# Optimization experiments

Hardware: AMD Instinct MI355X
Metric: run time of the kernel (lower is better)

## Reference

```python
import jax, jax.numpy as jnp
import numpy as np

N_ACT = 300000
C = 128
K = 9
BATCH, H, W = 4, 1024, 1024
EPS = 1e-4  # scn BatchNormalization default eps


def _build_rulebook(rng):
    # sample N_ACT unique active sites on a (BATCH, H, W) grid
    flat = np.sort(rng.choice(BATCH * H * W, size=N_ACT, replace=False).astype(np.int64))
    b = flat // (H * W)
    y = (flat // W) % H
    x = flat % W
    nbr = np.full((N_ACT, K), -1, dtype=np.int32)
    k = 0
    for dy in (-1, 0, 1):
        for dx in (-1, 0, 1):
            ny, nx = y + dy, x + dx
            valid = (ny >= 0) & (ny < H) & (nx >= 0) & (nx < W)
            nflat = b * (H * W) + ny * W + nx
            pos = np.searchsorted(flat, nflat)
            pos_c = np.clip(pos, 0, N_ACT - 1)
            found = valid & (flat[pos_c] == nflat)
            nbr[:, k] = np.where(found, pos_c, -1).astype(np.int32)
            k += 1
    return jnp.asarray(nbr)


def setup_inputs() -> dict:
    key = jax.random.key(0)
    k1, k2, k3 = jax.random.split(key, 3)
    rng = np.random.default_rng(0)
    nbr_idx = _build_rulebook(rng)
    scale = 1.0 / np.sqrt(K * C)
    return {
        "x": jax.random.normal(k1, (N_ACT, C), dtype=jnp.float32),
        "nbr_idx": nbr_idx,
        "W1": jax.random.normal(k2, (K, C, C), dtype=jnp.float32) * scale,
        "gamma1": jnp.ones((C,), jnp.float32),
        "beta1": jnp.zeros((C,), jnp.float32),
        "W2": jax.random.normal(k3, (K, C, C), dtype=jnp.float32) * scale,
        "gamma2": jnp.ones((C,), jnp.float32),
        "beta2": jnp.zeros((C,), jnp.float32),
    }


def _subm_conv(feats, nbr_idx, Wk):
    # gather -> GEMM -> accumulate, one pass per kernel offset (K=9 fixed)
    out = jnp.zeros((feats.shape[0], Wk.shape[2]), feats.dtype)
    for k in range(Wk.shape[0]):
        idx = nbr_idx[:, k]
        mask = (idx >= 0)[:, None]
        g = jnp.where(mask, feats[jnp.maximum(idx, 0)], 0.0)
        out = out + g @ Wk[k]
    return out


def _batchnorm(feats, gamma, beta):
    mean = feats.mean(axis=0)
    var = feats.var(axis=0)  # biased, as in torch BN normalization
    return (feats - mean) * jax.lax.rsqrt(var + EPS) * gamma + beta


def reference(x, nbr_idx, W1, gamma1, beta1, W2, gamma2, beta2):
    out = _subm_conv(x, nbr_idx, W1)
    out = jax.nn.relu(_batchnorm(out, gamma1, beta1))  # BatchNormReLU
    out = _subm_conv(out, nbr_idx, W2)
    out = _batchnorm(out, gamma2, beta2)  # BatchNormalization
    return jax.nn.relu(out + x)  # AddTable + ReLU
```

## Files before the change

kernel.cpp:

```cpp
#include <hip/hip_runtime.h>


#define N_ACT 300000
#define NTAP  9
#define EPSV  1e-4f

using f16x8 = __attribute__((ext_vector_type(8))) _Float16;
using f32x4 = __attribute__((ext_vector_type(4))) float;

#define OFF_PH    0UL
#define OFF_TMP   76800000UL
#define OFF_W1    230400000UL
#define OFF_W2    (OFF_W1 + 294912UL)
#define OFF_STATS (OFF_W2 + 294912UL)
#define OFF_ZBUF  (OFF_STATS + 2048UL)
#define OFF_SB    (OFF_ZBUF + 256UL)

__device__ __forceinline__ unsigned short f2h(float v) {
  _Float16 h = (_Float16)v;
  return __builtin_bit_cast(unsigned short, h);
}

__global__ void prep_kernel(const float* __restrict__ W1, const float* __restrict__ W2,
                            unsigned short* __restrict__ w1, unsigned short* __restrict__ w2,
                            float* __restrict__ zstats) {
  int b = blockIdx.x, t = threadIdx.x;
  if (b == 36) {
    for (int i = t; i < 576; i += 256) zstats[i] = 0.f;
    return;
  }
  int w = b / 18, rem = b % 18;
  int tap = rem >> 1, ch = rem & 1;
  const float* W = w ? W2 : W1;
  unsigned short* o = w ? w2 : w1;
  int n  = t >> 1;
  int s0 = (t & 1) * 4;
  for (int s = s0; s < s0 + 4; ++s) {
    int sigma = s ^ (n & 7);
    for (int j = 0; j < 8; ++j) {
      int   k = ch * 64 + sigma * 8 + j;
      float v = W[tap * 16384 + k * 128 + n];
      o[rem * 8192 + n * 64 + s * 8 + j] = f2h(v);
    }
  }
}

__global__ void tohalf_kernel(const float* __restrict__ x, unsigned short* __restrict__ ph) {
  int i = (blockIdx.x * 256 + threadIdx.x) * 8;
  float4 a = *(const float4*)(x + i);
  float4 b = *(const float4*)(x + i + 4);
  uint4 p;
  p.x = (unsigned)f2h(a.x) | ((unsigned)f2h(a.y) << 16);
  p.y = (unsigned)f2h(a.z) | ((unsigned)f2h(a.w) << 16);
  p.z = (unsigned)f2h(b.x) | ((unsigned)f2h(b.y) << 16);
  p.w = (unsigned)f2h(b.z) | ((unsigned)f2h(b.w) << 16);
  *(uint4*)(ph + i) = p;
}

__global__ __launch_bounds__(256, 4)
void conv_kernel(const unsigned short* __restrict__ pH, const int* __restrict__ nbr,
                 const unsigned short* __restrict__ wH,
                 float* __restrict__ outp, float* __restrict__ ssum, float* __restrict__ ssq,
                 const unsigned short* __restrict__ zbuf) {
  __shared__ char smem[32768];
  const int t  = threadIdx.x;
  const int wv = t >> 6, ln = t & 63;
  const int m0 = blockIdx.x * 128;
  const int rs = ln >> 3, sg = ln & 7;
  const int lane16 = ln & 15, g = ln >> 4;

  f32x4 acc[16];
#pragma unroll
  for (int i = 0; i < 16; ++i) acc[i] = f32x4{0.f, 0.f, 0.f, 0.f};

  for (int tap = 0; tap < NTAP; ++tap) {
    int idx4[4];
#pragma unroll
    for (int it = 0; it < 4; ++it) {
      int gm = m0 + wv * 32 + it * 8 + rs;
      idx4[it] = (gm < N_ACT) ? nbr[gm * 9 + tap] : -1;
    }
#pragma unroll
    for (int ch = 0; ch < 2; ++ch) {
      __syncthreads();
#pragma unroll
      for (int it = 0; it < 4; ++it) {
        int r     = wv * 32 + it * 8 + rs;
        int sigma = sg ^ (r & 7);
        int idx   = idx4[it];
        long off  = (long)(idx >= 0 ? idx : 0) * 128 + ch * 64 + sigma * 8;
        const unsigned short* gs = (idx >= 0) ? (pH + off) : (zbuf + sigma * 8);
        int lo = r * 128 + sg * 16;
        __builtin_amdgcn_global_load_lds((const __attribute__((address_space(1))) void*)gs,
                                         (__attribute__((address_space(3))) void*)(smem + lo), 16, 0, 0);
      }
      {
        const char* gb = (const char*)wH + (tap * 2 + ch) * 16384;
#pragma unroll
        for (int it = 0; it < 4; ++it) {
          int o = wv * 4096 + it * 1024 + ln * 16;
          __builtin_amdgcn_global_load_lds((const __attribute__((address_space(1))) void*)(gb + o),
                                           (__attribute__((address_space(3))) void*)(smem + 16384 + o), 16, 0, 0);
        }
      }
      __syncthreads();
#pragma unroll
      for (int ks = 0; ks < 2; ++ks) {
        f16x8 ah[4], bh[4];
        int sigma = ks * 4 + g;
#pragma unroll
        for (int mt = 0; mt < 4; ++mt) {
          int m = (wv & 1) * 64 + mt * 16 + lane16;
          ah[mt] = *(const f16x8*)(smem + m * 128 + ((sigma ^ (m & 7)) * 16));
        }
#pragma unroll
        for (int nt = 0; nt < 4; ++nt) {
          int n = (wv >> 1) * 64 + nt * 16 + lane16;
          bh[nt] = *(const f16x8*)(smem + 16384 + n * 128 + ((sigma ^ (n & 7)) * 16));
        }
#pragma unroll
        for (int mt = 0; mt < 4; ++mt)
#pragma unroll
          for (int nt = 0; nt < 4; ++nt)
            acc[mt * 4 + nt] = __builtin_amdgcn_mfma_f32_16x16x32_f16(ah[mt], bh[nt], acc[mt * 4 + nt], 0, 0, 0);
      }
    }
  }
  int rowbase = m0 + (wv & 1) * 64;
  int colbase = (wv >> 1) * 64;
  float s[4], q[4];
#pragma unroll
  for (int nt = 0; nt < 4; ++nt) { s[nt] = 0.f; q[nt] = 0.f; }
#pragma unroll
  for (int mt = 0; mt < 4; ++mt)
#pragma unroll
    for (int nt = 0; nt < 4; ++nt)
#pragma unroll
      for (int r = 0; r < 4; ++r) {
        float v  = acc[mt * 4 + nt][r];
        int  row = rowbase + mt * 16 + g * 4 + r;
        int  col = colbase + nt * 16 + lane16;
        if (row < N_ACT) outp[row * 128 + col] = v;
        s[nt] += v; q[nt] += v * v;
      }
  __syncthreads();
  float* sbuf = (float*)smem;
  float* qbuf = ((float*)smem) + 256;
#pragma unroll
  for (int nt = 0; nt < 4; ++nt) {
    float sv = s[nt], qv = q[nt];
    sv += __shfl_xor(sv, 16, 64); sv += __shfl_xor(sv, 32, 64);
    qv += __shfl_xor(qv, 16, 64); qv += __shfl_xor(qv, 32, 64);
    if (ln < 16) { sbuf[wv * 64 + nt * 16 + ln] = sv; qbuf[wv * 64 + nt * 16 + ln] = qv; }
  }
  __syncthreads();
  if (t < 128) {
    int c = t;
    float tot = (c < 64) ? (sbuf[c] + sbuf[64 + c]) : (sbuf[128 + (c - 64)] + sbuf[192 + (c - 64)]);
    atomicAdd(ssum + c, tot);
  } else {
    int c = t - 128;
    float tot = (c < 64) ? (qbuf[c] + qbuf[64 + c]) : (qbuf[128 + (c - 64)] + qbuf[192 + (c - 64)]);
    atomicAdd(ssq + c, tot);
  }
}

__global__ void finalize_stats_kernel(const float* __restrict__ ssum, const float* __restrict__ ssq,
                                      const float* __restrict__ gamma, const float* __restrict__ beta,
                                      float* __restrict__ scale, float* __restrict__ bias) {
  int c = threadIdx.x;
  float mean = ssum[c] * (1.f / N_ACT);
  float var  = ssq[c] * (1.f / N_ACT) - mean * mean;
  float sc   = rsqrtf(var + EPSV) * gamma[c];
  scale[c] = sc;
  bias[c]  = beta[c] - mean * sc;
}

__global__ void bn_relu_tohalf_kernel(const float* __restrict__ tmp,
                                      const float* __restrict__ scale, const float* __restrict__ bias,
                                      unsigned short* __restrict__ ph) {
  int i = (blockIdx.x * 256 + threadIdx.x) * 8;
  int c = i & 127;
  float4 v0 = *(const float4*)(tmp + i);
  float4 v1 = *(const float4*)(tmp + i + 4);
  float4 s0 = *(const float4*)(scale + c);
  float4 s1 = *(const float4*)(scale + c + 4);
  float4 b0 = *(const float4*)(bias + c);
  float4 b1 = *(const float4*)(bias + c + 4);
  float y0 = fmaxf(v0.x * s0.x + b0.x, 0.f);
  float y1 = fmaxf(v0.y * s0.y + b0.y, 0.f);
  float y2 = fmaxf(v0.z * s0.z + b0.z, 0.f);
  float y3 = fmaxf(v0.w * s0.w + b0.w, 0.f);
  float y4 = fmaxf(v1.x * s1.x + b1.x, 0.f);
  float y5 = fmaxf(v1.y * s1.y + b1.y, 0.f);
  float y6 = fmaxf(v1.z * s1.z + b1.z, 0.f);
  float y7 = fmaxf(v1.w * s1.w + b1.w, 0.f);
  uint4 p;
  p.x = (unsigned)f2h(y0) | ((unsigned)f2h(y1) << 16);
  p.y = (unsigned)f2h(y2) | ((unsigned)f2h(y3) << 16);
  p.z = (unsigned)f2h(y4) | ((unsigned)f2h(y5) << 16);
  p.w = (unsigned)f2h(y6) | ((unsigned)f2h(y7) << 16);
  *(uint4*)(ph + i) = p;
}

__global__ void final_kernel(const float* __restrict__ tmp,
                             const float* __restrict__ scale, const float* __restrict__ bias,
                             const float* __restrict__ x, float* __restrict__ outp) {
  int i = (blockIdx.x * 256 + threadIdx.x) * 4;
  int c = i & 127;
  float4 v  = *(const float4*)(tmp + i);
  float4 sc = *(const float4*)(scale + c);
  float4 bs = *(const float4*)(bias + c);
  float4 xx = *(const float4*)(x + i);
  float4 o;
  o.x = fmaxf(v.x * sc.x + bs.x + xx.x, 0.f);
  o.y = fmaxf(v.y * sc.y + bs.y + xx.y, 0.f);
  o.z = fmaxf(v.z * sc.z + bs.z + xx.z, 0.f);
  o.w = fmaxf(v.w * sc.w + bs.w + xx.w, 0.f);
  *(float4*)(outp + i) = o;
}

extern "C" void kernel_launch(void* const* d_in, const int* in_sizes, int n_in,
                              void* d_out, int out_size, void* d_ws, size_t ws_size,
                              hipStream_t stream) {
  const float* x   = (const float*)d_in[0];
  const int*   nbr = (const int*)d_in[1];
  const float* W1  = (const float*)d_in[2];
  const float* g1  = (const float*)d_in[3];
  const float* b1  = (const float*)d_in[4];
  const float* W2  = (const float*)d_in[5];
  const float* g2  = (const float*)d_in[6];
  const float* b2  = (const float*)d_in[7];
  float* out = (float*)d_out;
  char*  ws  = (char*)d_ws;

  unsigned short* ph  = (unsigned short*)(ws + OFF_PH);
  float*          tmp = (float*)(ws + OFF_TMP);
  unsigned short* w1  = (unsigned short*)(ws + OFF_W1);
  unsigned short* w2  = (unsigned short*)(ws + OFF_W2);
  float*          st  = (float*)(ws + OFF_STATS);
  unsigned short* zb  = (unsigned short*)(ws + OFF_ZBUF);
  float*          sc  = (float*)(ws + OFF_SB);
  float*          bi  = sc + 128;

  prep_kernel<<<37, 256, 0, stream>>>(W1, W2, w1, w2, st);
  tohalf_kernel<<<18750, 256, 0, stream>>>(x, ph);
  conv_kernel<<<2344, 256, 0, stream>>>(ph, nbr, w1, tmp, st, st + 128, zb);
  finalize_stats_kernel<<<1, 128, 0, stream>>>(st, st + 128, g1, b1, sc, bi);
  bn_relu_tohalf_kernel<<<18750, 256, 0, stream>>>(tmp, sc, bi, ph);
  conv_kernel<<<2344, 256, 0, stream>>>(ph, nbr, w2, tmp, st + 256, st + 384, zb);
  finalize_stats_kernel<<<1, 128, 0, stream>>>(st + 256, st + 384, g2, b2, sc, bi);
  final_kernel<<<37500, 256, 0, stream>>>(tmp, sc, bi, x, out);
}
```

Baseline: 592.6 us.

## Fuse fp16 conversion and BN+ReLU into conv gather, store fp16 intermediates

Removes the standalone tohalf and bn_relu_tohalf kernels by converting x to fp16 inside the first conv's gather and applying BN1+ReLU in fp16 on the fly in the second conv's gather. Conv outputs are stored as fp16 instead of fp32, which halves intermediate write and read traffic. Gathers now go through registers instead of async global_load_lds, and the first conv reads fp32 rows, doubling its gather bytes. Occupancy is lowered to 3 waves per SIMD, and doing BN in fp16 with half-precision outputs adds precision risk.

```diff
diff --git a/kernel.cpp b/kernel.cpp
--- a/kernel.cpp
+++ b/kernel.cpp
@@ -8,17 +8,20 @@
 using f16x8 = __attribute__((ext_vector_type(8))) _Float16;
 using f32x4 = __attribute__((ext_vector_type(4))) float;
 
-#define OFF_PH    0UL
-#define OFF_TMP   76800000UL
-#define OFF_W1    230400000UL
+#define OFF_T1    0UL
+#define OFF_T2    76800000UL
+#define OFF_W1    153600000UL
 #define OFF_W2    (OFF_W1 + 294912UL)
 #define OFF_STATS (OFF_W2 + 294912UL)
-#define OFF_ZBUF  (OFF_STATS + 2048UL)
-#define OFF_SB    (OFF_ZBUF + 256UL)
+#define OFF_SB1H  (OFF_STATS + 2048UL)
+#define OFF_SB2   (OFF_SB1H + 512UL)
 
 __device__ __forceinline__ unsigned short f2h(float v) {
   _Float16 h = (_Float16)v;
   return __builtin_bit_cast(unsigned short, h);
+}
+__device__ __forceinline__ float h2f(unsigned short u) {
+  return (float)__builtin_bit_cast(_Float16, u);
 }
 
 __global__ void prep_kernel(const float* __restrict__ W1, const float* __restrict__ W2,
@@ -26,7 +29,7 @@
                             float* __restrict__ zstats) {
   int b = blockIdx.x, t = threadIdx.x;
   if (b == 36) {
-    for (int i = t; i < 576; i += 256) zstats[i] = 0.f;
+    for (int i = t; i < 512; i += 256) zstats[i] = 0.f;
     return;
   }
   int w = b / 18, rem = b % 18;
@@ -39,35 +42,35 @@
     int sigma = s ^ (n & 7);
     for (int j = 0; j < 8; ++j) {
       int   k = ch * 64 + sigma * 8 + j;
-      float v = W[tap * 16384 + k * 128 + n];
-      o[rem * 8192 + n * 64 + s * 8 + j] = f2h(v);
+      o[rem * 8192 + n * 64 + s * 8 + j] = f2h(W[tap * 16384 + k * 128 + n]);
     }
   }
 }
 
-__global__ void tohalf_kernel(const float* __restrict__ x, unsigned short* __restrict__ ph) {
-  int i = (blockIdx.x * 256 + threadIdx.x) * 8;
-  float4 a = *(const float4*)(x + i);
-  float4 b = *(const float4*)(x + i + 4);
-  uint4 p;
-  p.x = (unsigned)f2h(a.x) | ((unsigned)f2h(a.y) << 16);
-  p.y = (unsigned)f2h(a.z) | ((unsigned)f2h(a.w) << 16);
-  p.z = (unsigned)f2h(b.x) | ((unsigned)f2h(b.y) << 16);
-  p.w = (unsigned)f2h(b.z) | ((unsigned)f2h(b.w) << 16);
-  *(uint4*)(ph + i) = p;
-}
-
-__global__ __launch_bounds__(256, 4)
-void conv_kernel(const unsigned short* __restrict__ pH, const int* __restrict__ nbr,
+template <int MODE>
+__global__ __launch_bounds__(256, 3)
+void conv_kernel(const void* __restrict__ srcv, const int* __restrict__ nbr,
                  const unsigned short* __restrict__ wH,
-                 float* __restrict__ outp, float* __restrict__ ssum, float* __restrict__ ssq,
-                 const unsigned short* __restrict__ zbuf) {
+                 const unsigned short* __restrict__ sbh,
+                 unsigned short* __restrict__ outp,
+                 float* __restrict__ ssum, float* __restrict__ ssq) {
   __shared__ char smem[32768];
   const int t  = threadIdx.x;
   const int wv = t >> 6, ln = t & 63;
   const int m0 = blockIdx.x * 128;
   const int rs = ln >> 3, sg = ln & 7;
   const int lane16 = ln & 15, g = ln >> 4;
+  const int sigma8 = (sg ^ rs) * 8;
+
+  const f16x8 zero8 = {0, 0, 0, 0, 0, 0, 0, 0};
+
+  f16x8 scv0 = zero8, scv1 = zero8, bsv0 = zero8, bsv1 = zero8;
+  if (MODE == 1) {
+    scv0 = *(const f16x8*)(sbh + sigma8);
+    scv1 = *(const f16x8*)(sbh + 64 + sigma8);
+    bsv0 = *(const f16x8*)(sbh + 128 + sigma8);
+    bsv1 = *(const f16x8*)(sbh + 192 + sigma8);
+  }
 
   f32x4 acc[16];
 #pragma unroll
@@ -85,14 +88,29 @@
       __syncthreads();
 #pragma unroll
       for (int it = 0; it < 4; ++it) {
-        int r     = wv * 32 + it * 8 + rs;
-        int sigma = sg ^ (r & 7);
-        int idx   = idx4[it];
-        long off  = (long)(idx >= 0 ? idx : 0) * 128 + ch * 64 + sigma * 8;
-        const unsigned short* gs = (idx >= 0) ? (pH + off) : (zbuf + sigma * 8);
-        int lo = r * 128 + sg * 16;
-        __builtin_amdgcn_global_load_lds((const __attribute__((address_space(1))) void*)gs,
-                                         (__attribute__((address_space(3))) void*)(smem + lo), 16, 0, 0);
+        int r   = wv * 32 + it * 8 + rs;
+        int idx = idx4[it];
+        long safe = (long)(idx < 0 ? 0 : idx);
+        f16x8 y;
+        if (MODE == 0) {
+          const float* s = (const float*)srcv + safe * 128 + ch * 64 + sigma8;
+          float4 a = *(const float4*)s;
+          float4 b = *(const float4*)(s + 4);
+          y[0] = (_Float16)a.x; y[1] = (_Float16)a.y; y[2] = (_Float16)a.z; y[3] = (_Float16)a.w;
+          y[4] = (_Float16)b.x; y[5] = (_Float16)b.y; y[6] = (_Float16)b.z; y[7] = (_Float16)b.w;
+        } else {
+          const unsigned short* s = (const unsigned short*)srcv + safe * 128 + ch * 64 + sigma8;
+          f16x8 v  = *(const f16x8*)s;
+          f16x8 sc = ch ? scv1 : scv0;
+          f16x8 bs = ch ? bsv1 : bsv0;
+#pragma unroll
+          for (int j = 0; j < 8; ++j) {
+            _Float16 z = v[j] * sc[j] + bs[j];
+            y[j] = z > (_Float16)0 ? z : (_Float16)0;
+          }
+        }
+        if (idx < 0) y = zero8;
+        *(f16x8*)(smem + r * 128 + sg * 16) = y;
       }
       {
         const char* gb = (const char*)wH + (tap * 2 + ch) * 16384;
@@ -140,7 +158,7 @@
         float v  = acc[mt * 4 + nt][r];
         int  row = rowbase + mt * 16 + g * 4 + r;
         int  col = colbase + nt * 16 + lane16;
-        if (row < N_ACT) outp[row * 128 + col] = v;
+        if (row < N_ACT) outp[row * 128 + col] = f2h(v);
         s[nt] += v; q[nt] += v * v;
       }
   __syncthreads();
@@ -165,9 +183,20 @@
   }
 }
 
-__global__ void finalize_stats_kernel(const float* __restrict__ ssum, const float* __restrict__ ssq,
-                                      const float* __restrict__ gamma, const float* __restrict__ beta,
-                                      float* __restrict__ scale, float* __restrict__ bias) {
+__global__ void finalize1_kernel(const float* __restrict__ ssum, const float* __restrict__ ssq,
+                                 const float* __restrict__ gamma, const float* __restrict__ beta,
+                                 unsigned short* __restrict__ sbh) {
+  int c = threadIdx.x;
+  float mean = ssum[c] * (1.f / N_ACT);
+  float var  = ssq[c] * (1.f / N_ACT) - mean * mean;
+  float sc   = rsqrtf(var + EPSV) * gamma[c];
+  sbh[c]       = f2h(sc);
+  sbh[128 + c] = f2h(beta[c] - mean * sc);
+}
+
+__global__ void finalize2_kernel(const float* __restrict__ ssum, const float* __restrict__ ssq,
+                                 const float* __restrict__ gamma, const float* __restrict__ beta,
+                                 float* __restrict__ scale, float* __restrict__ bias) {
   int c = threadIdx.x;
   float mean = ssum[c] * (1.f / N_ACT);
   float var  = ssq[c] * (1.f / N_ACT) - mean * mean;
@@ -176,47 +205,20 @@
   bias[c]  = beta[c] - mean * sc;
 }
 
-__global__ void bn_relu_tohalf_kernel(const float* __restrict__ tmp,
-                                      const float* __restrict__ scale, const float* __restrict__ bias,
-                                      unsigned short* __restrict__ ph) {
-  int i = (blockIdx.x * 256 + threadIdx.x) * 8;
-  int c = i & 127;
-  float4 v0 = *(const float4*)(tmp + i);
-  float4 v1 = *(const float4*)(tmp + i + 4);
-  float4 s0 = *(const float4*)(scale + c);
-  float4 s1 = *(const float4*)(scale + c + 4);
-  float4 b0 = *(const float4*)(bias + c);
-  float4 b1 = *(const float4*)(bias + c + 4);
-  float y0 = fmaxf(v0.x * s0.x + b0.x, 0.f);
-  float y1 = fmaxf(v0.y * s0.y + b0.y, 0.f);
-  float y2 = fmaxf(v0.z * s0.z + b0.z, 0.f);
-  float y3 = fmaxf(v0.w * s0.w + b0.w, 0.f);
-  float y4 = fmaxf(v1.x * s1.x + b1.x, 0.f);
-  float y5 = fmaxf(v1.y * s1.y + b1.y, 0.f);
-  float y6 = fmaxf(v1.z * s1.z + b1.z, 0.f);
-  float y7 = fmaxf(v1.w * s1.w + b1.w, 0.f);
-  uint4 p;
-  p.x = (unsigned)f2h(y0) | ((unsigned)f2h(y1) << 16);
-  p.y = (unsigned)f2h(y2) | ((unsigned)f2h(y3) << 16);
-  p.z = (unsigned)f2h(y4) | ((unsigned)f2h(y5) << 16);
-  p.w = (unsigned)f2h(y6) | ((unsigned)f2h(y7) << 16);
-  *(uint4*)(ph + i) = p;
-}
-
-__global__ void final_kernel(const float* __restrict__ tmp,
+__global__ void final_kernel(const unsigned short* __restrict__ t2,
                              const float* __restrict__ scale, const float* __restrict__ bias,
                              const float* __restrict__ x, float* __restrict__ outp) {
   int i = (blockIdx.x * 256 + threadIdx.x) * 4;
   int c = i & 127;
-  float4 v  = *(const float4*)(tmp + i);
-  float4 sc = *(const float4*)(scale + c);
-  float4 bs = *(const float4*)(bias + c);
-  float4 xx = *(const float4*)(x + i);
+  ushort4 hv = *(const ushort4*)(t2 + i);
+  float4 sc  = *(const float4*)(scale + c);
+  float4 bs  = *(const float4*)(bias + c);
+  float4 xx  = *(const float4*)(x + i);
   float4 o;
-  o.x = fmaxf(v.x * sc.x + bs.x + xx.x, 0.f);
-  o.y = fmaxf(v.y * sc.y + bs.y + xx.y, 0.f);
-  o.z = fmaxf(v.z * sc.z + bs.z + xx.z, 0.f);
-  o.w = fmaxf(v.w * sc.w + bs.w + xx.w, 0.f);
+  o.x = fmaxf(h2f(hv.x) * sc.x + bs.x + xx.x, 0.f);
+  o.y = fmaxf(h2f(hv.y) * sc.y + bs.y + xx.y, 0.f);
+  o.z = fmaxf(h2f(hv.z) * sc.z + bs.z + xx.z, 0.f);
+  o.w = fmaxf(h2f(hv.w) * sc.w + bs.w + xx.w, 0.f);
   *(float4*)(outp + i) = o;
 }
 
@@ -234,21 +236,19 @@
   float* out = (float*)d_out;
   char*  ws  = (char*)d_ws;
 
-  unsigned short* ph  = (unsigned short*)(ws + OFF_PH);
-  float*          tmp = (float*)(ws + OFF_TMP);
+  unsigned short* t1  = (unsigned short*)(ws + OFF_T1);
+  unsigned short* t2  = (unsigned short*)(ws + OFF_T2);
   unsigned short* w1  = (unsigned short*)(ws + OFF_W1);
   unsigned short* w2  = (unsigned short*)(ws + OFF_W2);
   float*          st  = (float*)(ws + OFF_STATS);
-  unsigned short* zb  = (unsigned short*)(ws + OFF_ZBUF);
-  float*          sc  = (float*)(ws + OFF_SB);
-  float*          bi  = sc + 128;
+  unsigned short* sbh = (unsigned short*)(ws + OFF_SB1H);
+  float*          sc2 = (float*)(ws + OFF_SB2);
+  float*          bs2 = sc2 + 128;
 
   prep_kernel<<<37, 256, 0, stream>>>(W1, W2, w1, w2, st);
-  tohalf_kernel<<<18750, 256, 0, stream>>>(x, ph);
-  conv_kernel<<<2344, 256, 0, stream>>>(ph, nbr, w1, tmp, st, st + 128, zb);
-  finalize_stats_kernel<<<1, 128, 0, stream>>>(st, st + 128, g1, b1, sc, bi);
-  bn_relu_tohalf_kernel<<<18750, 256, 0, stream>>>(tmp, sc, bi, ph);
-  conv_kernel<<<2344, 256, 0, stream>>>(ph, nbr, w2, tmp, st + 256, st + 384, zb);
-  finalize_stats_kernel<<<1, 128, 0, stream>>>(st + 256, st + 384, g2, b2, sc, bi);
-  final_kernel<<<37500, 256, 0, stream>>>(tmp, sc, bi, x, out);
-}
+  conv_kernel<0><<<2344, 256, 0, stream>>>(x, nbr, w1, nullptr, t1, st, st + 128);
+  finalize1_kernel<<<1, 128, 0, stream>>>(st, st + 128, g1, b1, sbh);
+  conv_kernel<1><<<2344, 256, 0, stream>>>(t1, nbr, w2, sbh, t2, st + 256, st + 384);
+  finalize2_kernel<<<1, 128, 0, stream>>>(st + 256, st + 384, g2, b2, sc2, bs2);
+  final_kernel<<<37500, 256, 0, stream>>>(t2, sc2, bs2, x, out);
+}
```

New measurement: 626.1 us. 5.6% more time.
